# Performance work log

Hardware: AMD Instinct MI355X
Metric: run time of the kernel (lower is better)

The kernel has to match this reference:

```python
import jax, jax.numpy as jnp
import numpy as np

B, N_IN, N_OUT = 16, 7000, 28000
C_IN, C_OUT, S = 64, 64, 9
NNZ = 3 * N_OUT  # ~3 source verts per upsampled vert (barycentric)


def setup_inputs() -> dict:
    key = jax.random.key(0)
    k = jax.random.split(key, 6)
    x = jax.random.normal(k[0], (B, N_IN, C_IN), dtype=jnp.float32)
    values = jax.random.uniform(k[1], (NNZ,), dtype=jnp.float32)
    row = jax.random.randint(k[2], (NNZ,), 0, N_OUT)
    col = jax.random.randint(k[3], (NNZ,), 0, N_IN)
    spiral_indices = jax.random.randint(k[4], (N_OUT, S), 0, N_OUT)
    weight = jax.random.normal(k[5], (S * C_IN, C_OUT), dtype=jnp.float32) * 0.02
    bias = jnp.zeros((C_OUT,), dtype=jnp.float32)
    return {"x": x, "values": values, "weight": weight, "bias": bias,
            "row": row, "col": col, "spiral_indices": spiral_indices}


def reference(x, values, weight, bias, row, col, spiral_indices):
    # Pool: gather source verts, scale by sparse matrix values, scatter-add to output verts
    n_out = spiral_indices.shape[0]
    gathered = x[:, col, :] * values[None, :, None]            # [B, nnz, C]
    pooled = jnp.zeros((x.shape[0], n_out, x.shape[2]), x.dtype).at[:, row, :].add(gathered)  # [B, N_out, C]
    # SpiralConv: gather spiral neighborhood, flatten, linear
    feat = pooled[:, spiral_indices.reshape(-1), :]            # [B, N_out*S, C]
    feat = feat.reshape(x.shape[0], n_out, -1)                 # [B, N_out, S*C]
    out = jax.nn.elu(jnp.einsum('bnf,fo->bno', feat, weight) + bias)
    return out
```

## Files before the change

### kernel.cpp

```cpp
#include <hip/hip_runtime.h>
#include <math.h>

#define B      16
#define N_IN   7000
#define N_OUT  28000
#define C      64
#define S      9
#define NNZ    (3 * N_OUT)
#define F      (S * C)
#define KB     (F / 32)

#define MT     110

typedef short bf16x8 __attribute__((ext_vector_type(8)));
typedef float f32x4  __attribute__((ext_vector_type(4)));

static __device__ __forceinline__ unsigned short f2bf(float f) {
    unsigned u = __float_as_uint(f);
    u += 0x7fffu + ((u >> 16) & 1u);
    return (unsigned short)(u >> 16);
}

__global__ void hist_kernel(const int* __restrict__ row, int* __restrict__ cnt) {
    int i = blockIdx.x * 256 + threadIdx.x;
    if (i < NNZ) atomicAdd(&cnt[row[i]], 1);
}

__global__ void scan_kernel(const int* __restrict__ cnt,
                            int* __restrict__ offs, int* __restrict__ cursor) {
    __shared__ int tmp[1024];
    const int t = threadIdx.x;
    const int base = t * 28;
    const bool live = (t < 1000);

    int c[28];
    int partial = 0;
    if (live) {
        #pragma unroll
        for (int j = 0; j < 28; ++j) { c[j] = cnt[base + j]; partial += c[j]; }
    }
    tmp[t] = partial;
    __syncthreads();
    #pragma unroll
    for (int off = 1; off < 1024; off <<= 1) {
        int v = (t >= off) ? tmp[t - off] : 0;
        __syncthreads();
        tmp[t] += v;
        __syncthreads();
    }
    if (live) {
        int run = tmp[t] - partial;
        #pragma unroll
        for (int j = 0; j < 28; ++j) {
            offs[base + j]   = run;
            cursor[base + j] = run;
            run += c[j];
        }
        if (t == 999) offs[N_OUT] = run;
    }
}

__global__ void place_kernel(const int* __restrict__ row, const int* __restrict__ col,
                             const float* __restrict__ values,
                             int* __restrict__ cursor,
                             int* __restrict__ ecol, float* __restrict__ eval) {
    int i = blockIdx.x * 256 + threadIdx.x;
    if (i < NNZ) {
        int pos = atomicAdd(&cursor[row[i]], 1);
        ecol[pos] = col[i];
        eval[pos] = values[i];
    }
}

__global__ void pool_kernel(const float* __restrict__ x,
                            const int*   __restrict__ ecol,
                            const float* __restrict__ eval,
                            const int*   __restrict__ offs,
                            unsigned short* __restrict__ pooled) {
    const int lane = threadIdx.x & 63;
    const int wave = threadIdx.x >> 6;
    const int r    = blockIdx.x * 4 + wave;
    const int g    = lane >> 4;
    const int sl   = lane & 15;

    const int start = offs[r], end = offs[r + 1];

    float4 acc[4];
    #pragma unroll
    for (int j = 0; j < 4; ++j) acc[j] = make_float4(0.f, 0.f, 0.f, 0.f);

    for (int e = start; e < end; ++e) {
        const int   cl = ecol[e];
        const float v  = eval[e];
        const float* basep = x + (size_t)cl * C + sl * 4;
        #pragma unroll
        for (int j = 0; j < 4; ++j) {
            const float4 xv = *(const float4*)(basep + (size_t)(g * 4 + j) * N_IN * C);
            acc[j].x = fmaf(xv.x, v, acc[j].x);
            acc[j].y = fmaf(xv.y, v, acc[j].y);
            acc[j].z = fmaf(xv.z, v, acc[j].z);
            acc[j].w = fmaf(xv.w, v, acc[j].w);
        }
    }
    #pragma unroll
    for (int j = 0; j < 4; ++j) {
        const int b = g * 4 + j;
        ushort4 o;
        o.x = f2bf(acc[j].x); o.y = f2bf(acc[j].y);
        o.z = f2bf(acc[j].z); o.w = f2bf(acc[j].w);
        *(ushort4*)(pooled + ((size_t)b * N_OUT + r) * C + sl * 4) = o;
    }
}

__global__ void packw_kernel(const float* __restrict__ w, unsigned short* __restrict__ pw) {
    const int kb   = blockIdx.x;
    const int nt   = threadIdx.x >> 6;
    const int lane = threadIdx.x & 63;
    const int lm   = lane & 15;
    const int quad = lane >> 4;

    unsigned short v[8];
    #pragma unroll
    for (int j = 0; j < 8; ++j) {
        const int k = kb * 32 + quad * 8 + j;
        const int n = nt * 16 + lm;
        v[j] = f2bf(w[(size_t)k * C + n]);
    }
    unsigned short* dst = pw + ((size_t)(kb * 4 + nt) * 64 + lane) * 8;
    #pragma unroll
    for (int j = 0; j < 8; ++j) dst[j] = v[j];
}

__global__ __launch_bounds__(256, 2)
void spiral_mfma(const unsigned short* __restrict__ pooled,
                 const bf16x8*         __restrict__ packedW,
                 const int*            __restrict__ sp,
                 const float*          __restrict__ bias,
                 float*                __restrict__ out) {
    const int L = blockIdx.x;
    int b, mtile;
    if (L < 8 * MT) { b = L & 7;                mtile = L >> 3; }
    else            { b = 8 + ((L - 8 * MT) & 7); mtile = (L - 8 * MT) >> 3; }

    const int wave = threadIdx.x >> 6;
    const int lane = threadIdx.x & 63;
    const int lm   = lane & 15;
    const int quad = lane >> 4;
    const int m_base = mtile * 256 + wave * 64;

    int spv[S];
    {
        int r = m_base + lane;
        if (r >= N_OUT) r = N_OUT - 1;
        #pragma unroll
        for (int s = 0; s < S; ++s) spv[s] = sp[r * S + s];
    }

    const unsigned short* poolb = pooled + (size_t)b * N_OUT * C;

    f32x4 acc[4][4];
    #pragma unroll
    for (int t = 0; t < 4; ++t)
        #pragma unroll
        for (int nt = 0; nt < 4; ++nt)
            acc[t][nt] = (f32x4){0.f, 0.f, 0.f, 0.f};

    int    rowi[2][4];
    bf16x8 abuf[2][2][4];
    bf16x8 bbuf[2][2][4];

    #pragma unroll
    for (int t = 0; t < 4; ++t)
        rowi[0][t] = __shfl(spv[0], t * 16 + lm, 64);
    #pragma unroll
    for (int half = 0; half < 2; ++half) {
        const int c0 = half * 32 + quad * 8;
        #pragma unroll
        for (int t = 0; t < 4; ++t)
            abuf[0][half][t] = *(const bf16x8*)(poolb + (size_t)rowi[0][t] * C + c0);
        #pragma unroll
        for (int nt = 0; nt < 4; ++nt)
            bbuf[0][half][nt] = packedW[(half * 4 + nt) * 64 + lane];
    }

    #pragma unroll
    for (int s = 0; s < S; ++s) {
        const int cur = s & 1, nxt = cur ^ 1;

        if (s + 1 < S) {
            #pragma unroll
            for (int t = 0; t < 4; ++t)
                rowi[nxt][t] = __shfl(spv[s + 1], t * 16 + lm, 64);
            #pragma unroll
            for (int half = 0; half < 2; ++half) {
                const int c0 = half * 32 + quad * 8;
                #pragma unroll
                for (int t = 0; t < 4; ++t)
                    abuf[nxt][half][t] =
                        *(const bf16x8*)(poolb + (size_t)rowi[nxt][t] * C + c0);
                #pragma unroll
                for (int nt = 0; nt < 4; ++nt)
                    bbuf[nxt][half][nt] =
                        packedW[(((s + 1) * 2 + half) * 4 + nt) * 64 + lane];
            }
        }

        #pragma unroll
        for (int half = 0; half < 2; ++half)
            #pragma unroll
            for (int nt = 0; nt < 4; ++nt)
                #pragma unroll
                for (int t = 0; t < 4; ++t)
                    acc[t][nt] = __builtin_amdgcn_mfma_f32_16x16x32_bf16(
                        abuf[cur][half][t], bbuf[cur][half][nt], acc[t][nt], 0, 0, 0);
    }

    #pragma unroll
    for (int nt = 0; nt < 4; ++nt) {
        const int n = nt * 16 + lm;
        const float bs = bias[n];
        #pragma unroll
        for (int t = 0; t < 4; ++t) {
            #pragma unroll
            for (int reg = 0; reg < 4; ++reg) {
                const int r = m_base + t * 16 + quad * 4 + reg;
                if (r < N_OUT) {
                    float v = acc[t][nt][reg] + bs;
                    v = v > 0.f ? v : (__expf(v) - 1.0f);
                    out[((size_t)b * N_OUT + r) * C + n] = v;
                }
            }
        }
    }
}

extern "C" void kernel_launch(void* const* d_in, const int* in_sizes, int n_in,
                              void* d_out, int out_size, void* d_ws, size_t ws_size,
                              hipStream_t stream) {
    const float* x      = (const float*)d_in[0];
    const float* values = (const float*)d_in[1];
    const float* weight = (const float*)d_in[2];
    const float* bias   = (const float*)d_in[3];
    const int*   row    = (const int*)d_in[4];
    const int*   col    = (const int*)d_in[5];
    const int*   sp     = (const int*)d_in[6];
    float*       out    = (float*)d_out;

    char* ws = (char*)d_ws;
    size_t off = 0;
    unsigned short* pooled  = (unsigned short*)(ws + off); off += (size_t)B * N_OUT * C * 2;
    unsigned short* packedW = (unsigned short*)(ws + off); off += (size_t)KB * 4 * 64 * 8 * 2;
    int*   offs   = (int*)(ws + off); off += ((size_t)(N_OUT + 1) * 4 + 124) / 128 * 128;
    int*   cursor = (int*)(ws + off); off += (size_t)N_OUT * 4 + 128;
    int*   cnt    = (int*)(ws + off); off += (size_t)N_OUT * 4 + 128;
    int*   ecol   = (int*)(ws + off); off += (size_t)NNZ * 4;
    float* eval   = (float*)(ws + off); off += (size_t)NNZ * 4;

    (void)hipMemsetAsync(cnt, 0, (size_t)N_OUT * 4, stream);
    hist_kernel <<<(NNZ + 255) / 256, 256, 0, stream>>>(row, cnt);
    scan_kernel <<<1, 1024, 0, stream>>>(cnt, offs, cursor);
    place_kernel<<<(NNZ + 255) / 256, 256, 0, stream>>>(row, col, values, cursor, ecol, eval);

    packw_kernel<<<KB, 256, 0, stream>>>(weight, packedW);

    pool_kernel<<<N_OUT / 4, 256, 0, stream>>>(x, ecol, eval, offs, pooled);

    spiral_mfma<<<B * MT, 256, 0, stream>>>(pooled,
        reinterpret_cast<const bf16x8*>(packedW), sp, bias, out);
}
```

Measured before the change: 324.9 us.

## Shrink spiral MFMA tile and regroup pool kernel by batch group

The spiral GEMM kernel now covers 32 rows per wave instead of 64, halving the accumulator and A-fragment registers. Weight fragments are loaded each step instead of double-buffered, and launch bounds are raised to 4 blocks per CU for more latency hiding on the gathers. The pool kernel is remapped so each block handles 8 rows for a fixed group of 8 batches, with every lane doing one batch and row, to improve locality of x gathers per batch. In exchange, weight loads are no longer prefetched and more blocks are launched.

```diff
diff --git a/kernel.cpp b/kernel.cpp
--- a/kernel.cpp
+++ b/kernel.cpp
@@ -10,7 +10,7 @@
 #define F      (S * C)
 #define KB     (F / 32)
 
-#define MT     110
+#define MT     219
 
 typedef short bf16x8 __attribute__((ext_vector_type(8)));
 typedef float f32x4  __attribute__((ext_vector_type(4)));
@@ -77,39 +77,36 @@
                             const float* __restrict__ eval,
                             const int*   __restrict__ offs,
                             unsigned short* __restrict__ pooled) {
+    const int bg     = blockIdx.x & 7;
+    const int rowblk = blockIdx.x >> 3;
+    const int wave = threadIdx.x >> 6;
     const int lane = threadIdx.x & 63;
-    const int wave = threadIdx.x >> 6;
-    const int r    = blockIdx.x * 4 + wave;
-    const int g    = lane >> 4;
+    const int rsub = lane >> 5;
+    const int bsub = (lane >> 4) & 1;
     const int sl   = lane & 15;
 
+    const int r = rowblk * 8 + wave * 2 + rsub;
+    const int b = bg + 8 * bsub;
+
     const int start = offs[r], end = offs[r + 1];
 
-    float4 acc[4];
-    #pragma unroll
-    for (int j = 0; j < 4; ++j) acc[j] = make_float4(0.f, 0.f, 0.f, 0.f);
+    float4 acc = make_float4(0.f, 0.f, 0.f, 0.f);
+    const float* xb = x + (size_t)b * N_IN * C + sl * 4;
 
     for (int e = start; e < end; ++e) {
         const int   cl = ecol[e];
         const float v  = eval[e];
-        const float* basep = x + (size_t)cl * C + sl * 4;
-        #pragma unroll
-        for (int j = 0; j < 4; ++j) {
-            const float4 xv = *(const float4*)(basep + (size_t)(g * 4 + j) * N_IN * C);
-            acc[j].x = fmaf(xv.x, v, acc[j].x);
-            acc[j].y = fmaf(xv.y, v, acc[j].y);
-            acc[j].z = fmaf(xv.z, v, acc[j].z);
-            acc[j].w = fmaf(xv.w, v, acc[j].w);
-        }
-    }
-    #pragma unroll
-    for (int j = 0; j < 4; ++j) {
-        const int b = g * 4 + j;
-        ushort4 o;
-        o.x = f2bf(acc[j].x); o.y = f2bf(acc[j].y);
-        o.z = f2bf(acc[j].z); o.w = f2bf(acc[j].w);
-        *(ushort4*)(pooled + ((size_t)b * N_OUT + r) * C + sl * 4) = o;
-    }
+        const float4 xv = *(const float4*)(xb + (size_t)cl * C);
+        acc.x = fmaf(xv.x, v, acc.x);
+        acc.y = fmaf(xv.y, v, acc.y);
+        acc.z = fmaf(xv.z, v, acc.z);
+        acc.w = fmaf(xv.w, v, acc.w);
+    }
+
+    ushort4 o;
+    o.x = f2bf(acc.x); o.y = f2bf(acc.y);
+    o.z = f2bf(acc.z); o.w = f2bf(acc.w);
+    *(ushort4*)(pooled + ((size_t)b * N_OUT + r) * C + sl * 4) = o;
 }
 
 __global__ void packw_kernel(const float* __restrict__ w, unsigned short* __restrict__ pw) {
@@ -131,7 +128,7 @@
     for (int j = 0; j < 8; ++j) dst[j] = v[j];
 }
 
-__global__ __launch_bounds__(256, 2)
+__global__ __launch_bounds__(256, 4)
 void spiral_mfma(const unsigned short* __restrict__ pooled,
                  const bf16x8*         __restrict__ packedW,
                  const int*            __restrict__ sp,
@@ -139,18 +136,18 @@
                  float*                __restrict__ out) {
     const int L = blockIdx.x;
     int b, mtile;
-    if (L < 8 * MT) { b = L & 7;                mtile = L >> 3; }
+    if (L < 8 * MT) { b = L & 7;                  mtile = L >> 3; }
     else            { b = 8 + ((L - 8 * MT) & 7); mtile = (L - 8 * MT) >> 3; }
 
     const int wave = threadIdx.x >> 6;
     const int lane = threadIdx.x & 63;
     const int lm   = lane & 15;
     const int quad = lane >> 4;
-    const int m_base = mtile * 256 + wave * 64;
+    const int m_base = mtile * 128 + wave * 32;
 
     int spv[S];
     {
-        int r = m_base + lane;
+        int r = m_base + (lane & 31);
         if (r >= N_OUT) r = N_OUT - 1;
         #pragma unroll
         for (int s = 0; s < S; ++s) spv[s] = sp[r * S + s];
@@ -158,50 +155,49 @@
 
     const unsigned short* poolb = pooled + (size_t)b * N_OUT * C;
 
-    f32x4 acc[4][4];
-    #pragma unroll
-    for (int t = 0; t < 4; ++t)
+    f32x4 acc[2][4];
+    #pragma unroll
+    for (int t = 0; t < 2; ++t)
         #pragma unroll
         for (int nt = 0; nt < 4; ++nt)
             acc[t][nt] = (f32x4){0.f, 0.f, 0.f, 0.f};
 
-    int    rowi[2][4];
-    bf16x8 abuf[2][2][4];
-    bf16x8 bbuf[2][2][4];
-
-    #pragma unroll
-    for (int t = 0; t < 4; ++t)
+    int    rowi[2][2];
+    bf16x8 abuf[2][2][2];
+
+    #pragma unroll
+    for (int t = 0; t < 2; ++t)
         rowi[0][t] = __shfl(spv[0], t * 16 + lm, 64);
     #pragma unroll
     for (int half = 0; half < 2; ++half) {
         const int c0 = half * 32 + quad * 8;
         #pragma unroll
-        for (int t = 0; t < 4; ++t)
+        for (int t = 0; t < 2; ++t)
             abuf[0][half][t] = *(const bf16x8*)(poolb + (size_t)rowi[0][t] * C + c0);
-        #pragma unroll
-        for (int nt = 0; nt < 4; ++nt)
-            bbuf[0][half][nt] = packedW[(half * 4 + nt) * 64 + lane];
     }
 
     #pragma unroll
     for (int s = 0; s < S; ++s) {
         const int cur = s & 1, nxt = cur ^ 1;
 
+        bf16x8 bbuf[2][4];
+        #pragma unroll
+        for (int half = 0; half < 2; ++half)
+            #pragma unroll
+            for (int nt = 0; nt < 4; ++nt)
+                bbuf[half][nt] = packedW[((s * 2 + half) * 4 + nt) * 64 + lane];
+
         if (s + 1 < S) {
             #pragma unroll
-            for (int t = 0; t < 4; ++t)
+            for (int t = 0; t < 2; ++t)
                 rowi[nxt][t] = __shfl(spv[s + 1], t * 16 + lm, 64);
             #pragma unroll
             for (int half = 0; half < 2; ++half) {
                 const int c0 = half * 32 + quad * 8;
                 #pragma unroll
-                for (int t = 0; t < 4; ++t)
+                for (int t = 0; t < 2; ++t)
                     abuf[nxt][half][t] =
                         *(const bf16x8*)(poolb + (size_t)rowi[nxt][t] * C + c0);
-                #pragma unroll
-                for (int nt = 0; nt < 4; ++nt)
-                    bbuf[nxt][half][nt] =
-                        packedW[(((s + 1) * 2 + half) * 4 + nt) * 64 + lane];
             }
         }
 
@@ -210,9 +206,9 @@
             #pragma unroll
             for (int nt = 0; nt < 4; ++nt)
                 #pragma unroll
-                for (int t = 0; t < 4; ++t)
+                for (int t = 0; t < 2; ++t)
                     acc[t][nt] = __builtin_amdgcn_mfma_f32_16x16x32_bf16(
-                        abuf[cur][half][t], bbuf[cur][half][nt], acc[t][nt], 0, 0, 0);
+                        abuf[cur][half][t], bbuf[half][nt], acc[t][nt], 0, 0, 0);
     }
 
     #pragma unroll
@@ -220,7 +216,7 @@
         const int n = nt * 16 + lm;
         const float bs = bias[n];
         #pragma unroll
-        for (int t = 0; t < 4; ++t) {
+        for (int t = 0; t < 2; ++t) {
             #pragma unroll
             for (int reg = 0; reg < 4; ++reg) {
                 const int r = m_base + t * 16 + quad * 4 + reg;
@@ -263,7 +259,7 @@
 
     packw_kernel<<<KB, 256, 0, stream>>>(weight, packedW);
 
-    pool_kernel<<<N_OUT / 4, 256, 0, stream>>>(x, ecol, eval, offs, pooled);
+    pool_kernel<<<(N_OUT / 8) * 8, 256, 0, stream>>>(x, ecol, eval, offs, pooled);
 
     spiral_mfma<<<B * MT, 256, 0, stream>>>(pooled,
         reinterpret_cast<const bf16x8*>(packedW), sp, bias, out);
```

Result: no change. 319.7 us (-1.6%).
